# Optimization experiments

Hardware: AMD Instinct MI355X
Metric: run time of the kernel (lower is better)

Reference implementation:

```python
import jax, jax.numpy as jnp
import numpy as np

B, S, D, E, K = 4, 4096, 2048, 16, 2
TEMPERATURE = 1.0


def setup_inputs() -> dict:
    key = jax.random.key(0)
    ks = jax.random.split(key, 4)
    scale = 1.0 / np.sqrt(D)
    return {
        "x": jax.random.normal(ks[0], (B, S, D), dtype=jnp.float32),
        "w_route": jax.random.normal(ks[1], (D, E), dtype=jnp.float32) * scale,
        "b_route": jnp.zeros((E,), dtype=jnp.float32),
        "w_noise": jax.random.normal(ks[2], (D, E), dtype=jnp.float32) * scale,
        "b_noise": jnp.zeros((E,), dtype=jnp.float32),
        "eps": jax.random.normal(ks[3], (B, S, E), dtype=jnp.float32),
    }


def reference(x, w_route, b_route, w_noise, b_noise, eps):
    # dual linear projections: (B,S,D) @ (D,E) -> (B,S,E)
    logits = jnp.einsum("bsd,de->bse", x, w_route) + b_route
    noise_logits = jnp.einsum("bsd,de->bse", x, w_noise) + b_noise
    noise_scale = jax.nn.softplus(noise_logits)
    scaled_logits = (logits + eps * noise_scale) / TEMPERATURE

    top_k_logits, indices = jax.lax.top_k(scaled_logits, K)  # (B,S,K)
    # scatter top-k back over -inf, equivalent to masking non-topk entries
    in_topk = jax.nn.one_hot(indices, E, dtype=jnp.bool_).any(axis=-2)  # (B,S,E)
    sparse_logits = jnp.where(in_topk, scaled_logits, -jnp.inf)
    router_output = jax.nn.softmax(sparse_logits, axis=-1)

    router_prob = router_output.mean(axis=(0, 1))
    target = 1.0 / E
    aux_loss = jnp.sum((router_prob - target) ** 2)
    return router_output, indices, aux_loss
```

## Files before the change

### kernel.cpp

```cpp
#include <hip/hip_runtime.h>
#include <math.h>


#define DDIM 2048
#define NEXP 16
#define RPB 32
#define WAVE_D 256
#define NCH 16
#define NGRP 64
#define RED_OFF 8192
#define IDX_OFF 262144
#define AUX_OFF 294912
#define NBLK 512

__global__ __launch_bounds__(512, 4) void router_main_k(
    const float* __restrict__ x, const float* __restrict__ wr,
    const float* __restrict__ br, const float* __restrict__ wn,
    const float* __restrict__ bn, const float* __restrict__ eps,
    float* __restrict__ out, float* __restrict__ wsp) {
  __shared__ float smem[8 * 1024 + 32 * 36];

  const int tid  = threadIdx.x;
  const int wave = tid >> 6;
  const int lane = tid & 63;
  const int rg   = lane >> 3;
  const int q    = lane & 7;
  const int q4   = q * 4;
  const int row_base = blockIdx.x * RPB;

  float* xregion = smem + wave * 1024;

  const int sr  = lane & 31;
  const int sc0 = (lane >> 5) * 2;
  const float* xg = x + (size_t)(row_base + sr) * DDIM + wave * WAVE_D + sc0 * 4;
  const int ls0 = sr * 16 + (((sc0    ) ^ (sr & 3)) << 2);
  const int ls1 = sr * 16 + (((sc0 ^ 1) ^ (sr & 3)) << 2);

  const float* wbase = (q < 4 ? wr : wn) + (size_t)(wave * WAVE_D) * NEXP + (q4 & 15);

  float4 acc[4];
  #pragma unroll
  for (int i = 0; i < 4; ++i) acc[i] = make_float4(0.f, 0.f, 0.f, 0.f);

  float4 wp[2][4];
  float4 xp0, xp1;

  #pragma unroll
  for (int j = 0; j < 4; ++j) wp[0][j] = *(const float4*)(wbase + j * NEXP);
  xp0 = *(const float4*)(xg);
  xp1 = *(const float4*)(xg + 4);
  *(float4*)(xregion + ls0) = xp0;
  *(float4*)(xregion + ls1) = xp1;

  const int swr = rg & 3;

  for (int k = 0; k < NCH; ++k) {
    const float* xb = xregion + (k & 1) * 512;
    #pragma unroll
    for (int gg = 0; gg < 4; ++gg) {
      const int G = (k << 2) + gg;
      const int P = gg & 1;
      if (G + 1 < NGRP) {
        const float* wl = wbase + (size_t)(G + 1) * 4 * NEXP;
        #pragma unroll
        for (int j = 0; j < 4; ++j) wp[P ^ 1][j] = *(const float4*)(wl + j * NEXP);
      }
      if (gg == 0 && k + 1 < NCH) {
        xp0 = *(const float4*)(xg + (k + 1) * 16);
        xp1 = *(const float4*)(xg + (k + 1) * 16 + 4);
      }
      #pragma unroll
      for (int i = 0; i < 4; ++i) {
        const float4 xv = *(const float4*)(xb + ((rg + 8 * i) << 4) + ((gg ^ swr) << 2));
        acc[i].x = fmaf(xv.w, wp[P][3].x, fmaf(xv.z, wp[P][2].x, fmaf(xv.y, wp[P][1].x, fmaf(xv.x, wp[P][0].x, acc[i].x))));
        acc[i].y = fmaf(xv.w, wp[P][3].y, fmaf(xv.z, wp[P][2].y, fmaf(xv.y, wp[P][1].y, fmaf(xv.x, wp[P][0].y, acc[i].y))));
        acc[i].z = fmaf(xv.w, wp[P][3].z, fmaf(xv.z, wp[P][2].z, fmaf(xv.y, wp[P][1].z, fmaf(xv.x, wp[P][0].z, acc[i].z))));
        acc[i].w = fmaf(xv.w, wp[P][3].w, fmaf(xv.z, wp[P][2].w, fmaf(xv.y, wp[P][1].w, fmaf(xv.x, wp[P][0].w, acc[i].w))));
      }
      if (gg == 3 && k + 1 < NCH) {
        float* xw = xregion + ((k + 1) & 1) * 512;
        *(float4*)(xw + ls0) = xp0;
        *(float4*)(xw + ls1) = xp1;
      }
    }
  }

  {
    float* pr = xregion;
    const int psw = (q ^ rg) << 2;
    #pragma unroll
    for (int i = 0; i < 4; ++i)
      *(float4*)(pr + ((rg + 8 * i) << 5) + psw) = acc[i];
  }
  __syncthreads();

  if (tid < 256) {
    const int row = tid >> 3;
    const int g   = tid & 7;
    const int rsw = (g ^ (row & 7)) << 2;
    float4 s = make_float4(0.f, 0.f, 0.f, 0.f);
    #pragma unroll
    for (int w = 0; w < 8; ++w) {
      float4 a = *(const float4*)(smem + (w << 10) + (row << 5) + rsw);
      s.x += a.x; s.y += a.y; s.z += a.z; s.w += a.w;
    }
    *(float4*)(smem + RED_OFF + row * 36 + g * 4) = s;
  }
  __syncthreads();

  if (tid < RPB) {
    const int row_l = tid;
    const int row_g = row_base + row_l;
    float c[32];
    #pragma unroll
    for (int g = 0; g < 8; ++g) {
      float4 a = *(const float4*)(smem + RED_OFF + row_l * 36 + g * 4);
      c[g * 4 + 0] = a.x; c[g * 4 + 1] = a.y; c[g * 4 + 2] = a.z; c[g * 4 + 3] = a.w;
    }

    float brv[16], bnv[16], ev[16];
    #pragma unroll
    for (int g = 0; g < 4; ++g) {
      *(float4*)(brv + g * 4) = *(const float4*)(br + g * 4);
      *(float4*)(bnv + g * 4) = *(const float4*)(bn + g * 4);
      *(float4*)(ev  + g * 4) = *(const float4*)(eps + (size_t)row_g * NEXP + g * 4);
    }

    float s[16];
    #pragma unroll
    for (int e = 0; e < 16; ++e) {
      float lg = c[e] + brv[e];
      float nz = c[16 + e] + bnv[e];
      float sp = fmaxf(nz, 0.f) + log1pf(expf(-fabsf(nz)));
      s[e] = lg + ev[e] * sp;
    }

    float b1 = s[0]; int i1 = 0;
    #pragma unroll
    for (int e = 1; e < 16; ++e) { if (s[e] > b1) { b1 = s[e]; i1 = e; } }
    float b2 = -INFINITY; int i2 = 0;
    #pragma unroll
    for (int e = 0; e < 16; ++e) { if (e != i1 && s[e] > b2) { b2 = s[e]; i2 = e; } }

    float t2 = expf(b2 - b1);
    float p1 = 1.f / (1.f + t2);
    float p2 = t2 / (1.f + t2);

    float v[16];
    #pragma unroll
    for (int e = 0; e < 16; ++e)
      v[e] = (e == i1) ? p1 : ((e == i2) ? p2 : 0.f);

    float* orow = out + (size_t)row_g * NEXP;
    *(float4*)(orow + 0)  = make_float4(v[0], v[1], v[2], v[3]);
    *(float4*)(orow + 4)  = make_float4(v[4], v[5], v[6], v[7]);
    *(float4*)(orow + 8)  = make_float4(v[8], v[9], v[10], v[11]);
    *(float4*)(orow + 12) = make_float4(v[12], v[13], v[14], v[15]);

    float* oidx = out + IDX_OFF + (size_t)row_g * 2;
    *(float2*)oidx = make_float2((float)i1, (float)i2);

    #pragma unroll
    for (int m = 1; m < 32; m <<= 1) {
      #pragma unroll
      for (int e = 0; e < 16; ++e) v[e] += __shfl_xor(v[e], m, 32);
    }
    if (tid == 0) {
      float* wp2 = wsp + (size_t)blockIdx.x * 16;
      *(float4*)(wp2 + 0)  = make_float4(v[0], v[1], v[2], v[3]);
      *(float4*)(wp2 + 4)  = make_float4(v[4], v[5], v[6], v[7]);
      *(float4*)(wp2 + 8)  = make_float4(v[8], v[9], v[10], v[11]);
      *(float4*)(wp2 + 12) = make_float4(v[12], v[13], v[14], v[15]);
    }
  }
}

__global__ void router_aux_k(const float* __restrict__ wsp, float* __restrict__ out_aux) {
  __shared__ float red[16][17];
  __shared__ float sq[16];
  const int t = threadIdx.x;
  const int e = t & 15;
  const int g = t >> 4;
  float ssum = 0.f;
  for (int b = 0; b < 32; ++b) ssum += wsp[(size_t)(g * 32 + b) * 16 + e];
  red[g][e] = ssum;
  __syncthreads();
  if (t < 16) {
    float tot = 0.f;
    #pragma unroll
    for (int gg = 0; gg < 16; ++gg) tot += red[gg][t];
    float diff = tot * (1.f / 16384.f) - 0.0625f;
    sq[t] = diff * diff;
  }
  __syncthreads();
  if (t == 0) {
    float a = 0.f;
    #pragma unroll
    for (int i = 0; i < 16; ++i) a += sq[i];
    *out_aux = a;
  }
}

extern "C" void kernel_launch(void* const* d_in, const int* in_sizes, int n_in,
                              void* d_out, int out_size, void* d_ws, size_t ws_size,
                              hipStream_t stream) {
  const float* x   = (const float*)d_in[0];
  const float* wr  = (const float*)d_in[1];
  const float* br  = (const float*)d_in[2];
  const float* wn  = (const float*)d_in[3];
  const float* bn  = (const float*)d_in[4];
  const float* eps = (const float*)d_in[5];
  float* out = (float*)d_out;
  float* wsp = (float*)d_ws;

  router_main_k<<<NBLK, 512, 0, stream>>>(x, wr, br, wn, bn, eps, out, wsp);
  router_aux_k<<<1, 256, 0, stream>>>(wsp, out + AUX_OFF);
}
```

Baseline: 64.45 us.

## Double rows per block, split D across 16 waves, tree-reduce partials

```diff
diff --git a/kernel.cpp b/kernel.cpp
--- a/kernel.cpp
+++ b/kernel.cpp
@@ -4,80 +4,74 @@
 
 #define DDIM 2048
 #define NEXP 16
-#define RPB 32
-#define WAVE_D 256
-#define NCH 16
-#define NGRP 64
-#define RED_OFF 8192
+#define RPB 64
+#define WAVE_D 128
+#define NCHNK 16
+#define NGRP 32
 #define IDX_OFF 262144
 #define AUX_OFF 294912
-#define NBLK 512
-
-__global__ __launch_bounds__(512, 4) void router_main_k(
+#define NBLK 256
+
+__global__ __launch_bounds__(1024, 4) void router_main_k(
     const float* __restrict__ x, const float* __restrict__ wr,
     const float* __restrict__ br, const float* __restrict__ wn,
     const float* __restrict__ bn, const float* __restrict__ eps,
     float* __restrict__ out, float* __restrict__ wsp) {
-  __shared__ float smem[8 * 1024 + 32 * 36];
+  __shared__ float smem[16384];
 
   const int tid  = threadIdx.x;
   const int wave = tid >> 6;
   const int lane = tid & 63;
   const int rg   = lane >> 3;
   const int q    = lane & 7;
-  const int q4   = q * 4;
   const int row_base = blockIdx.x * RPB;
 
   float* xregion = smem + wave * 1024;
 
-  const int sr  = lane & 31;
-  const int sc0 = (lane >> 5) * 2;
-  const float* xg = x + (size_t)(row_base + sr) * DDIM + wave * WAVE_D + sc0 * 4;
-  const int ls0 = sr * 16 + (((sc0    ) ^ (sr & 3)) << 2);
-  const int ls1 = sr * 16 + (((sc0 ^ 1) ^ (sr & 3)) << 2);
-
-  const float* wbase = (q < 4 ? wr : wn) + (size_t)(wave * WAVE_D) * NEXP + (q4 & 15);
-
-  float4 acc[4];
+  const float* xg0 = x + (size_t)(row_base + (lane >> 1)) * DDIM + wave * WAVE_D + (lane & 1) * 4;
+  const float* xg1 = xg0 + (size_t)32 * DDIM;
+  const int ls0 = lane * 4;
+  const int ls1 = lane * 4 + 256;
+
+  const float* wbase = (q < 4 ? wr : wn) + (size_t)(wave * WAVE_D) * NEXP + (q & 3) * 4;
+
+  float4 acc[8];
   #pragma unroll
-  for (int i = 0; i < 4; ++i) acc[i] = make_float4(0.f, 0.f, 0.f, 0.f);
+  for (int i = 0; i < 8; ++i) acc[i] = make_float4(0.f, 0.f, 0.f, 0.f);
 
   float4 wp[2][4];
   float4 xp0, xp1;
 
   #pragma unroll
   for (int j = 0; j < 4; ++j) wp[0][j] = *(const float4*)(wbase + j * NEXP);
-  xp0 = *(const float4*)(xg);
-  xp1 = *(const float4*)(xg + 4);
+  xp0 = *(const float4*)(xg0);
+  xp1 = *(const float4*)(xg1);
   *(float4*)(xregion + ls0) = xp0;
   *(float4*)(xregion + ls1) = xp1;
 
-  const int swr = rg & 3;
-
-  for (int k = 0; k < NCH; ++k) {
+  for (int k = 0; k < NCHNK; ++k) {
     const float* xb = xregion + (k & 1) * 512;
     #pragma unroll
-    for (int gg = 0; gg < 4; ++gg) {
-      const int G = (k << 2) + gg;
-      const int P = gg & 1;
+    for (int gg = 0; gg < 2; ++gg) {
+      const int G = (k << 1) + gg;
       if (G + 1 < NGRP) {
         const float* wl = wbase + (size_t)(G + 1) * 4 * NEXP;
         #pragma unroll
-        for (int j = 0; j < 4; ++j) wp[P ^ 1][j] = *(const float4*)(wl + j * NEXP);
-      }
-      if (gg == 0 && k + 1 < NCH) {
-        xp0 = *(const float4*)(xg + (k + 1) * 16);
-        xp1 = *(const float4*)(xg + (k + 1) * 16 + 4);
+        for (int j = 0; j < 4; ++j) wp[gg ^ 1][j] = *(const float4*)(wl + j * NEXP);
+      }
+      if (gg == 0 && k + 1 < NCHNK) {
+        xp0 = *(const float4*)(xg0 + (k + 1) * 8);
+        xp1 = *(const float4*)(xg1 + (k + 1) * 8);
       }
       #pragma unroll
-      for (int i = 0; i < 4; ++i) {
-        const float4 xv = *(const float4*)(xb + ((rg + 8 * i) << 4) + ((gg ^ swr) << 2));
-        acc[i].x = fmaf(xv.w, wp[P][3].x, fmaf(xv.z, wp[P][2].x, fmaf(xv.y, wp[P][1].x, fmaf(xv.x, wp[P][0].x, acc[i].x))));
-        acc[i].y = fmaf(xv.w, wp[P][3].y, fmaf(xv.z, wp[P][2].y, fmaf(xv.y, wp[P][1].y, fmaf(xv.x, wp[P][0].y, acc[i].y))));
-        acc[i].z = fmaf(xv.w, wp[P][3].z, fmaf(xv.z, wp[P][2].z, fmaf(xv.y, wp[P][1].z, fmaf(xv.x, wp[P][0].z, acc[i].z))));
-        acc[i].w = fmaf(xv.w, wp[P][3].w, fmaf(xv.z, wp[P][2].w, fmaf(xv.y, wp[P][1].w, fmaf(xv.x, wp[P][0].w, acc[i].w))));
-      }
-      if (gg == 3 && k + 1 < NCH) {
+      for (int i = 0; i < 8; ++i) {
+        const float4 xv = *(const float4*)(xb + (rg + 8 * i) * 8 + (gg << 2));
+        acc[i].x = fmaf(xv.w, wp[gg][3].x, fmaf(xv.z, wp[gg][2].x, fmaf(xv.y, wp[gg][1].x, fmaf(xv.x, wp[gg][0].x, acc[i].x))));
+        acc[i].y = fmaf(xv.w, wp[gg][3].y, fmaf(xv.z, wp[gg][2].y, fmaf(xv.y, wp[gg][1].y, fmaf(xv.x, wp[gg][0].y, acc[i].y))));
+        acc[i].z = fmaf(xv.w, wp[gg][3].z, fmaf(xv.z, wp[gg][2].z, fmaf(xv.y, wp[gg][1].z, fmaf(xv.x, wp[gg][0].z, acc[i].z))));
+        acc[i].w = fmaf(xv.w, wp[gg][3].w, fmaf(xv.z, wp[gg][2].w, fmaf(xv.y, wp[gg][1].w, fmaf(xv.x, wp[gg][0].w, acc[i].w))));
+      }
+      if (gg == 1 && k + 1 < NCHNK) {
         float* xw = xregion + ((k + 1) & 1) * 512;
         *(float4*)(xw + ls0) = xp0;
         *(float4*)(xw + ls1) = xp1;
@@ -85,36 +79,42 @@
     }
   }
 
-  {
-    float* pr = xregion;
-    const int psw = (q ^ rg) << 2;
-    #pragma unroll
-    for (int i = 0; i < 4; ++i)
-      *(float4*)(pr + ((rg + 8 * i) << 5) + psw) = acc[i];
-  }
-  __syncthreads();
-
-  if (tid < 256) {
-    const int row = tid >> 3;
-    const int g   = tid & 7;
-    const int rsw = (g ^ (row & 7)) << 2;
-    float4 s = make_float4(0.f, 0.f, 0.f, 0.f);
-    #pragma unroll
-    for (int w = 0; w < 8; ++w) {
-      float4 a = *(const float4*)(smem + (w << 10) + (row << 5) + rsw);
-      s.x += a.x; s.y += a.y; s.z += a.z; s.w += a.w;
-    }
-    *(float4*)(smem + RED_OFF + row * 36 + g * 4) = s;
-  }
-  __syncthreads();
-
-  if (tid < RPB) {
-    const int row_l = tid;
+  const int psw = (q ^ rg) << 2;
+
+#define DUMP_R(Rg) { float* pr = smem + (Rg) * 2048; \
+    _Pragma("unroll") for (int i = 0; i < 8; ++i) \
+      *(float4*)(pr + (rg + 8 * i) * 32 + psw) = acc[i]; }
+#define ADD_R(Rg) { const float* pr = smem + (Rg) * 2048; \
+    _Pragma("unroll") for (int i = 0; i < 8; ++i) { \
+      float4 a = *(const float4*)(pr + (rg + 8 * i) * 32 + psw); \
+      acc[i].x += a.x; acc[i].y += a.y; acc[i].z += a.z; acc[i].w += a.w; } }
+
+  __syncthreads();
+  if (wave >= 8) DUMP_R(wave - 8);
+  __syncthreads();
+  if (wave < 8)  ADD_R(wave);
+  __syncthreads();
+  if (wave >= 4 && wave < 8) DUMP_R(wave - 4);
+  __syncthreads();
+  if (wave < 4)  ADD_R(wave);
+  __syncthreads();
+  if (wave >= 2 && wave < 4) DUMP_R(wave - 2);
+  __syncthreads();
+  if (wave < 2)  ADD_R(wave);
+  __syncthreads();
+  if (wave == 1) DUMP_R(0);
+  __syncthreads();
+
+  if (wave == 0) {
+    ADD_R(0);
+    DUMP_R(0);
+
+    const int row_l = lane;
     const int row_g = row_base + row_l;
     float c[32];
     #pragma unroll
     for (int g = 0; g < 8; ++g) {
-      float4 a = *(const float4*)(smem + RED_OFF + row_l * 36 + g * 4);
+      float4 a = *(const float4*)(smem + row_l * 32 + ((g ^ (row_l & 7)) << 2));
       c[g * 4 + 0] = a.x; c[g * 4 + 1] = a.y; c[g * 4 + 2] = a.z; c[g * 4 + 3] = a.w;
     }
 
@@ -161,16 +161,16 @@
     *(float2*)oidx = make_float2((float)i1, (float)i2);
 
     #pragma unroll
-    for (int m = 1; m < 32; m <<= 1) {
+    for (int m = 1; m < 64; m <<= 1) {
       #pragma unroll
-      for (int e = 0; e < 16; ++e) v[e] += __shfl_xor(v[e], m, 32);
-    }
-    if (tid == 0) {
-      float* wp2 = wsp + (size_t)blockIdx.x * 16;
-      *(float4*)(wp2 + 0)  = make_float4(v[0], v[1], v[2], v[3]);
-      *(float4*)(wp2 + 4)  = make_float4(v[4], v[5], v[6], v[7]);
-      *(float4*)(wp2 + 8)  = make_float4(v[8], v[9], v[10], v[11]);
-      *(float4*)(wp2 + 12) = make_float4(v[12], v[13], v[14], v[15]);
+      for (int e = 0; e < 16; ++e) v[e] += __shfl_xor(v[e], m, 64);
+    }
+    if (lane == 0) {
+      float* wpo = wsp + (size_t)blockIdx.x * 16;
+      *(float4*)(wpo + 0)  = make_float4(v[0], v[1], v[2], v[3]);
+      *(float4*)(wpo + 4)  = make_float4(v[4], v[5], v[6], v[7]);
+      *(float4*)(wpo + 8)  = make_float4(v[8], v[9], v[10], v[11]);
+      *(float4*)(wpo + 12) = make_float4(v[12], v[13], v[14], v[15]);
     }
   }
 }
@@ -182,7 +182,8 @@
   const int e = t & 15;
   const int g = t >> 4;
   float ssum = 0.f;
-  for (int b = 0; b < 32; ++b) ssum += wsp[(size_t)(g * 32 + b) * 16 + e];
+  #pragma unroll
+  for (int b = 0; b < 16; ++b) ssum += wsp[(size_t)(g * 16 + b) * 16 + e];
   red[g][e] = ssum;
   __syncthreads();
   if (t < 16) {
@@ -213,6 +214,6 @@
   float* out = (float*)d_out;
   float* wsp = (float*)d_ws;
 
-  router_main_k<<<NBLK, 512, 0, stream>>>(x, wr, br, wn, bn, eps, out, wsp);
+  router_main_k<<<NBLK, 1024, 0, stream>>>(x, wr, br, wn, bn, eps, out, wsp);
   router_aux_k<<<1, 256, 0, stream>>>(wsp, out + AUX_OFF);
 }
```

Result: slower. 96.26 us (+49.4%).
